# Optimization experiments

Hardware: AMD Instinct MI355X
Metric: run time of the kernel (lower is better)

The kernel has to match this reference:

```python
import jax, jax.numpy as jnp
import numpy as np

T_SCALES = [0.0, 0.25, 0.5, 0.75, 1.0]  # ODEblock time_scales; Euler step per consecutive pair
NUM_ZEROS = 10
BETA = 0.6  # defined in ODEFunc but unused in its forward


def _odefunc(x, x0, adj, alpha, w, d, w2, d2):
    # x: [B, N, T, Fa]; adj: [N, N]; alpha: [N]; w: [Fa, Fa]; d: [Fa]; w2: [T, T]; d2: [T]
    a = jax.nn.sigmoid(alpha)[None, :, None, None]              # [1, N, 1, 1]
    xa = jnp.einsum('ij,kjln->kiln', adj, x)                    # adjacency propagation over nodes
    dc = jnp.clip(d, 0.0, 1.0)
    W = (w * dc) @ w.T                                          # [Fa, Fa]
    # NOTE: faithful to torch source: 'ijkl,mn->ijkm' has NO shared contraction
    # index => xw = (sum_l x) outer (sum_n W) — reproduced exactly.
    xw = jnp.einsum('ijkl,mn->ijkm', x, W)
    d2c = jnp.clip(d2, 0.0, 1.0)
    W2 = (w2 * d2c) @ w2.T                                      # [T, T]
    xw2 = jnp.einsum('ijkl,kn->ijnl', x, W2)                    # temporal mixing
    # f = alpha/2*xa - x + xw - x + xw2 - x + x0
    return a * 0.5 * xa - 3.0 * x + xw + xw2 + x0


def setup_inputs() -> dict:
    key = jax.random.key(0)
    k1, k2 = jax.random.split(key)
    B, N, T, F = 32, 512, 24, 64
    Fa = F + NUM_ZEROS
    x = jax.random.normal(k1, (B, N, T, F), dtype=jnp.float32)
    adj = jax.random.uniform(k2, (N, N), dtype=jnp.float32) / N  # normalized dense adjacency
    alpha = 0.8 * jnp.ones((N,), jnp.float32)                    # nn.Parameter init 0.8*ones
    w = jnp.eye(Fa, dtype=jnp.float32)                           # nn.Parameter init eye
    d = jnp.ones((Fa,), jnp.float32)                             # nn.Parameter init ones
    w2 = jnp.eye(T, dtype=jnp.float32)
    d2 = jnp.ones((T,), jnp.float32)
    return {"x": x, "adj": adj, "alpha": alpha, "w": w, "d": d, "w2": w2, "d2": d2}


def reference(x, adj, alpha, w, d, w2, d2):
    B, N, T, F = x.shape
    if F == 64:
        x_aug = jnp.concatenate(
            [x, jnp.zeros((B, N, T, NUM_ZEROS), dtype=x.dtype)], axis=3)
    else:
        x_aug = x
    x0 = jax.lax.stop_gradient(x_aug)  # set_x0 uses clone().detach()
    # Euler odeint with two time points does one step: z = x + dt * f(x).
    # Original loop restarts from x_aug each iteration, so f is constant.
    f = _odefunc(x_aug, x0, adj, alpha, w, d, w2, d2)
    z = x_aug
    for i in range(len(T_SCALES) - 1):
        dt = T_SCALES[i + 1] - T_SCALES[i]
        z = x_aug + dt * f  # overwrites z each iteration, as in the torch code
    return jax.nn.relu(z)
```

## Files before the change

### kernel.cpp

```cpp
#include <hip/hip_runtime.h>
#include <hip/hip_bf16.h>
#include <cstdint>
#include <cstddef>

#define B_  32
#define N_  512
#define T_  24
#define F_  64
#define FA_ 74
#define NC  1536

typedef __attribute__((ext_vector_type(8))) short short8;
typedef __attribute__((ext_vector_type(4))) float floatx4;

#define WS_ADJB 1536
#define WS_XT   132608

#define AS1(p) ((const __attribute__((address_space(1))) void*)(p))
#define AS3(p) ((__attribute__((address_space(3))) void*)(p))

__global__ __launch_bounds__(256) void params_kernel(
    const float* __restrict__ alpha, const float* __restrict__ w,
    const float* __restrict__ d, const float* __restrict__ w2,
    const float* __restrict__ d2, float* __restrict__ ws) {
  __shared__ float cs[FA_];
  int tid = threadIdx.x;
  if (tid < FA_) {
    float s = 0.f;
    for (int n = 0; n < FA_; ++n) s += w[n * FA_ + tid];
    cs[tid] = s;
  }
  __syncthreads();
  if (tid < FA_) {
    float s = 0.f;
    for (int p = 0; p < FA_; ++p) {
      float dc = fminf(fmaxf(d[p], 0.f), 1.f);
      s += w[tid * FA_ + p] * dc * cs[p];
    }
    ws[tid] = s;
  }
  for (int e = tid; e < T_ * T_; e += 256) {
    int a = e / T_, b = e % T_;
    float s = 0.f;
    for (int p = 0; p < T_; ++p) {
      float dc = fminf(fmaxf(d2[p], 0.f), 1.f);
      s += w2[a * T_ + p] * dc * w2[b * T_ + p];
    }
    ws[128 + e] = s;
  }
  for (int i = tid; i < N_; i += 256) ws[768 + i] = 1.f / (1.f + __expf(-alpha[i]));
}

__global__ __launch_bounds__(256) void convert_adj_kernel(
    const float* __restrict__ adj, float* __restrict__ ws) {
  __hip_bfloat16* adjB = (__hip_bfloat16*)(ws + WS_ADJB);
  int g = (blockIdx.x * 256 + threadIdx.x) * 4;
  float4 v = *(const float4*)&adj[g];
  ushort4 u;
  __hip_bfloat16 h;
  h = __float2bfloat16(v.x); u.x = *(unsigned short*)&h;
  h = __float2bfloat16(v.y); u.y = *(unsigned short*)&h;
  h = __float2bfloat16(v.z); u.z = *(unsigned short*)&h;
  h = __float2bfloat16(v.w); u.w = *(unsigned short*)&h;
  *(ushort4*)&adjB[g] = u;
}

__global__ __launch_bounds__(256) void transpose_x_kernel(
    const float* __restrict__ x, float* __restrict__ ws) {
  __hip_bfloat16* xT = (__hip_bfloat16*)(ws + WS_XT);
  __shared__ float tile[64 * 65];
  int tid = threadIdx.x;
  int b = blockIdx.z;
  int c0 = blockIdx.x * 64;
  int k0 = blockIdx.y * 64;
#pragma unroll
  for (int it = 0; it < 4; ++it) {
    int g = it * 256 + tid;
    int k = g >> 4, c4 = g & 15;
    float4 v = *(const float4*)&x[((size_t)(b * N_ + k0 + k)) * NC + c0 + c4 * 4];
    tile[k * 65 + c4 * 4 + 0] = v.x;
    tile[k * 65 + c4 * 4 + 1] = v.y;
    tile[k * 65 + c4 * 4 + 2] = v.z;
    tile[k * 65 + c4 * 4 + 3] = v.w;
  }
  __syncthreads();
#pragma unroll
  for (int it = 0; it < 4; ++it) {
    int h = it * 256 + tid;
    int c = h >> 4, k4 = h & 15;
    ushort4 u;
    __hip_bfloat16 hb;
    hb = __float2bfloat16(tile[(k4 * 4 + 0) * 65 + c]); u.x = *(unsigned short*)&hb;
    hb = __float2bfloat16(tile[(k4 * 4 + 1) * 65 + c]); u.y = *(unsigned short*)&hb;
    hb = __float2bfloat16(tile[(k4 * 4 + 2) * 65 + c]); u.z = *(unsigned short*)&hb;
    hb = __float2bfloat16(tile[(k4 * 4 + 3) * 65 + c]); u.w = *(unsigned short*)&hb;
    *(ushort4*)&xT[((size_t)b * NC + c0 + c) * 512 + k0 + k4 * 4] = u;
  }
}

__global__ __launch_bounds__(256) void pass1_kernel(
    const float* __restrict__ x, const float* __restrict__ ws, float* __restrict__ out) {
  __shared__ float xs[4 * T_ * FA_];
  __shared__ float Ss[4 * T_];
  __shared__ float rsWs[80];
  int tid = threadIdx.x;
  int blk = blockIdx.x;
  int b = blk >> 7;
  int i0 = (blk & 127) << 2;
  const float* xb = x + (size_t)(b * N_ + i0) * NC;

  if (tid < FA_) rsWs[tid] = ws[tid];
#pragma unroll
  for (int it = 0; it < 6; ++it) {
    int g = it * 256 + tid;
    *(float4*)&xs[g * 4] = *(const float4*)&xb[g * 4];
  }
  __syncthreads();

  int node = tid >> 6, f = tid & 63;
  float xcol[24];
#pragma unroll
  for (int t = 0; t < 24; ++t) xcol[t] = xs[node * 1536 + t * 64 + f];
  __syncthreads();

  float S[24];
#pragma unroll
  for (int t = 0; t < 24; ++t) S[t] = xcol[t];
#pragma unroll
  for (int off = 32; off >= 1; off >>= 1) {
#pragma unroll
    for (int t = 0; t < 24; ++t) S[t] += __shfl_xor(S[t], off, 64);
  }
  if ((tid & 63) == 0) {
#pragma unroll
    for (int t = 0; t < 24; ++t) Ss[node * 24 + t] = S[t];
  }

  const float* __restrict__ W2p = ws + 128;
  float accv[24];
#pragma unroll
  for (int to = 0; to < 24; ++to) {
    float a = 0.f;
#pragma unroll
    for (int tp = 0; tp < 24; ++tp) a += xcol[tp] * W2p[to * 24 + tp];
    accv[to] = a;
  }
  float rsWf = rsWs[f];
#pragma unroll
  for (int t = 0; t < 24; ++t) {
    float val = 0.5f * xcol[t] + 0.25f * S[t] * rsWf + 0.25f * accv[t];
    xs[node * 1776 + t * 74 + f] = val;
  }
  __syncthreads();

#pragma unroll
  for (int it = 0; it < 4; ++it) {
    int e = it * 256 + tid;
    if (e < 960) {
      int nd = e / 240;
      int rem = e - nd * 240;
      int t = rem / 10;
      int m = rem - t * 10;
      float val = 0.25f * Ss[nd * 24 + t] * rsWs[64 + m];
      xs[nd * 1776 + t * 74 + 64 + m] = fmaxf(val, 0.f);
    }
  }
  __syncthreads();

  float* outb = out + (size_t)(b * N_ + i0) * 1776;
#pragma unroll
  for (int it = 0; it < 7; ++it) {
    int g = it * 256 + tid;
    if (g < 1776) *(float4*)&outb[g * 4] = *(float4*)&xs[g * 4];
  }
}

__global__ __launch_bounds__(256) void gemm_kernel(
    const float* __restrict__ ws, float* __restrict__ out) {
  const unsigned short* adjB = (const unsigned short*)(ws + WS_ADJB);
  const unsigned short* xT   = (const unsigned short*)(ws + WS_XT);
  __shared__ short As[128 * 32];
  __shared__ short Bs[128 * 32];

  int tid = threadIdx.x;
  int b  = blockIdx.z;
  int i0 = blockIdx.y * 128;
  int c0 = blockIdx.x * 128;
  int wave = tid >> 6, lane = tid & 63;
  int mw = (wave & 1) * 64, nw = (wave >> 1) * 64;
  int l15 = lane & 15, l4 = lane >> 4;

  floatx4 acc[4][4];
#pragma unroll
  for (int mt = 0; mt < 4; ++mt)
#pragma unroll
    for (int nt = 0; nt < 4; ++nt) acc[mt][nt] = (floatx4){0.f, 0.f, 0.f, 0.f};

  const size_t bRow = (size_t)b * NC;
  for (int k0 = 0; k0 < 512; k0 += 32) {
#pragma unroll
    for (int rep = 0; rep < 2; ++rep) {
      int chunk = rep * 256 + tid;
      int r = chunk >> 2;
      int k8 = (chunk & 3) * 8;
      __builtin_amdgcn_global_load_lds(AS1(adjB + (size_t)(i0 + r) * 512 + k0 + k8),
                                       AS3(&As[chunk * 8]), 16, 0, 0);
      __builtin_amdgcn_global_load_lds(AS1(xT + (bRow + c0 + r) * 512 + k0 + k8),
                                       AS3(&Bs[chunk * 8]), 16, 0, 0);
    }
    __syncthreads();

    short8 af[4], bf[4];
#pragma unroll
    for (int mt = 0; mt < 4; ++mt)
      af[mt] = *(const short8*)&As[(mw + mt * 16 + l15) * 32 + l4 * 8];
#pragma unroll
    for (int nt = 0; nt < 4; ++nt)
      bf[nt] = *(const short8*)&Bs[(nw + nt * 16 + l15) * 32 + l4 * 8];
#pragma unroll
    for (int mt = 0; mt < 4; ++mt)
#pragma unroll
      for (int nt = 0; nt < 4; ++nt)
        acc[mt][nt] = __builtin_amdgcn_mfma_f32_16x16x32_bf16(af[mt], bf[nt], acc[mt][nt], 0, 0, 0);
    __syncthreads();
  }

  float coeff[4][4];
#pragma unroll
  for (int mt = 0; mt < 4; ++mt)
#pragma unroll
    for (int r = 0; r < 4; ++r)
      coeff[mt][r] = 0.125f * ws[768 + i0 + mw + mt * 16 + l4 * 4 + r];

#pragma unroll
  for (int mt = 0; mt < 4; ++mt) {
#pragma unroll
    for (int nt = 0; nt < 4; ++nt) {
      int col = c0 + nw + nt * 16 + l15;
      int t = col >> 6, f = col & 63;
#pragma unroll
      for (int r = 0; r < 4; ++r) {
        int row = i0 + mw + mt * 16 + l4 * 4 + r;
        size_t o = ((size_t)(b * N_ + row) * T_ + t) * FA_ + f;
        float val = out[o] + coeff[mt][r] * acc[mt][nt][r];
        out[o] = fmaxf(val, 0.f);
      }
    }
  }
}

extern "C" void kernel_launch(void* const* d_in, const int* in_sizes, int n_in,
                              void* d_out, int out_size, void* d_ws, size_t ws_size,
                              hipStream_t stream) {
  const float* x     = (const float*)d_in[0];
  const float* adj   = (const float*)d_in[1];
  const float* alpha = (const float*)d_in[2];
  const float* w     = (const float*)d_in[3];
  const float* d     = (const float*)d_in[4];
  const float* w2    = (const float*)d_in[5];
  const float* d2    = (const float*)d_in[6];
  float* out = (float*)d_out;
  float* ws  = (float*)d_ws;

  hipLaunchKernelGGL(params_kernel, dim3(1), dim3(256), 0, stream,
                     alpha, w, d, w2, d2, ws);
  hipLaunchKernelGGL(convert_adj_kernel, dim3(256), dim3(256), 0, stream, adj, ws);
  hipLaunchKernelGGL(transpose_x_kernel, dim3(24, 8, B_), dim3(256), 0, stream, x, ws);
  hipLaunchKernelGGL(pass1_kernel, dim3(B_ * (N_ / 4)), dim3(256), 0, stream, x, ws, out);
  hipLaunchKernelGGL(gemm_kernel, dim3(12, 4, B_), dim3(256), 0, stream, ws, out);
}
```

Baseline: 345.5 us.

## Fuse x transpose with elementwise pass and stage bf16 epilogue buffer

Merges the x transpose and the per-node elementwise pass into one prep kernel, so x is read once, converted to bf16 and written both transposed for the GEMM and as a bf16 epilogue term. The sigmoid(alpha)/8 row scale is folded into the bf16 adjacency conversion, which removes the coefficient load in the GEMM epilogue. When the workspace is large enough, the GEMM epilogue reads a bf16 E buffer instead of doing a read-modify-write on the fp32 output. This cuts global traffic but adds bf16 rounding to the residual terms, and launches fewer blocks (32x32) per prep pass.

```diff
diff --git a/kernel.cpp b/kernel.cpp
--- a/kernel.cpp
+++ b/kernel.cpp
@@ -9,15 +9,26 @@
 #define F_  64
 #define FA_ 74
 #define NC  1536
+#define NCF 1776
 
 typedef __attribute__((ext_vector_type(8))) short short8;
 typedef __attribute__((ext_vector_type(4))) float floatx4;
 
-#define WS_ADJB 1536
+#define WS_ADJ  1536
 #define WS_XT   132608
+#define WS_E    12715520
+#define WS_BYTES_NEEDED (27264512ULL * 4ULL)
 
 #define AS1(p) ((const __attribute__((address_space(1))) void*)(p))
 #define AS3(p) ((__attribute__((address_space(3))) void*)(p))
+
+__device__ __forceinline__ unsigned short f2b(float v) {
+  __hip_bfloat16 h = __float2bfloat16(v);
+  return *(unsigned short*)&h;
+}
+__device__ __forceinline__ float b2f(unsigned short u) {
+  return __uint_as_float(((unsigned)u) << 16);
+}
 
 __global__ __launch_bounds__(256) void params_kernel(
     const float* __restrict__ alpha, const float* __restrict__ w,
@@ -53,131 +64,132 @@
 
 __global__ __launch_bounds__(256) void convert_adj_kernel(
     const float* __restrict__ adj, float* __restrict__ ws) {
-  __hip_bfloat16* adjB = (__hip_bfloat16*)(ws + WS_ADJB);
+  unsigned short* adjM = (unsigned short*)(ws + WS_ADJ);
   int g = (blockIdx.x * 256 + threadIdx.x) * 4;
+  int i = g >> 9;
+  float s = 0.125f * ws[768 + i];
   float4 v = *(const float4*)&adj[g];
   ushort4 u;
-  __hip_bfloat16 h;
-  h = __float2bfloat16(v.x); u.x = *(unsigned short*)&h;
-  h = __float2bfloat16(v.y); u.y = *(unsigned short*)&h;
-  h = __float2bfloat16(v.z); u.z = *(unsigned short*)&h;
-  h = __float2bfloat16(v.w); u.w = *(unsigned short*)&h;
-  *(ushort4*)&adjB[g] = u;
-}
-
-__global__ __launch_bounds__(256) void transpose_x_kernel(
-    const float* __restrict__ x, float* __restrict__ ws) {
-  __hip_bfloat16* xT = (__hip_bfloat16*)(ws + WS_XT);
-  __shared__ float tile[64 * 65];
+  u.x = f2b(s * v.x); u.y = f2b(s * v.y); u.z = f2b(s * v.z); u.w = f2b(s * v.w);
+  *(ushort4*)&adjM[g] = u;
+}
+
+template <bool EPATH>
+__global__ __launch_bounds__(256) void prep_kernel(
+    const float* __restrict__ x, float* __restrict__ ws, float* __restrict__ out) {
+  __shared__ __align__(16) unsigned short xsh[16 * NC];
+  __shared__ __align__(16) float ebuf[4 * NCF];
+  unsigned short* eh = (unsigned short*)ebuf;
+
   int tid = threadIdx.x;
-  int b = blockIdx.z;
-  int c0 = blockIdx.x * 64;
-  int k0 = blockIdx.y * 64;
-#pragma unroll
-  for (int it = 0; it < 4; ++it) {
+  int b = blockIdx.y;
+  int i0 = blockIdx.x * 16;
+  const float* xb = x + ((size_t)(b * N_ + i0)) * NC;
+
+#pragma unroll
+  for (int it = 0; it < 24; ++it) {
     int g = it * 256 + tid;
-    int k = g >> 4, c4 = g & 15;
-    float4 v = *(const float4*)&x[((size_t)(b * N_ + k0 + k)) * NC + c0 + c4 * 4];
-    tile[k * 65 + c4 * 4 + 0] = v.x;
-    tile[k * 65 + c4 * 4 + 1] = v.y;
-    tile[k * 65 + c4 * 4 + 2] = v.z;
-    tile[k * 65 + c4 * 4 + 3] = v.w;
+    float4 v = *(const float4*)&xb[g * 4];
+    ushort4 u;
+    u.x = f2b(v.x); u.y = f2b(v.y); u.z = f2b(v.z); u.w = f2b(v.w);
+    *(ushort4*)&xsh[g * 4] = u;
   }
   __syncthreads();
-#pragma unroll
-  for (int it = 0; it < 4; ++it) {
-    int h = it * 256 + tid;
-    int c = h >> 4, k4 = h & 15;
-    ushort4 u;
-    __hip_bfloat16 hb;
-    hb = __float2bfloat16(tile[(k4 * 4 + 0) * 65 + c]); u.x = *(unsigned short*)&hb;
-    hb = __float2bfloat16(tile[(k4 * 4 + 1) * 65 + c]); u.y = *(unsigned short*)&hb;
-    hb = __float2bfloat16(tile[(k4 * 4 + 2) * 65 + c]); u.z = *(unsigned short*)&hb;
-    hb = __float2bfloat16(tile[(k4 * 4 + 3) * 65 + c]); u.w = *(unsigned short*)&hb;
-    *(ushort4*)&xT[((size_t)b * NC + c0 + c) * 512 + k0 + k4 * 4] = u;
-  }
-}
-
-__global__ __launch_bounds__(256) void pass1_kernel(
-    const float* __restrict__ x, const float* __restrict__ ws, float* __restrict__ out) {
-  __shared__ float xs[4 * T_ * FA_];
-  __shared__ float Ss[4 * T_];
-  __shared__ float rsWs[80];
-  int tid = threadIdx.x;
-  int blk = blockIdx.x;
-  int b = blk >> 7;
-  int i0 = (blk & 127) << 2;
-  const float* xb = x + (size_t)(b * N_ + i0) * NC;
-
-  if (tid < FA_) rsWs[tid] = ws[tid];
-#pragma unroll
-  for (int it = 0; it < 6; ++it) {
-    int g = it * 256 + tid;
-    *(float4*)&xs[g * 4] = *(const float4*)&xb[g * 4];
-  }
-  __syncthreads();
-
-  int node = tid >> 6, f = tid & 63;
-  float xcol[24];
-#pragma unroll
-  for (int t = 0; t < 24; ++t) xcol[t] = xs[node * 1536 + t * 64 + f];
-  __syncthreads();
-
-  float S[24];
-#pragma unroll
-  for (int t = 0; t < 24; ++t) S[t] = xcol[t];
-#pragma unroll
-  for (int off = 32; off >= 1; off >>= 1) {
-#pragma unroll
-    for (int t = 0; t < 24; ++t) S[t] += __shfl_xor(S[t], off, 64);
-  }
-  if ((tid & 63) == 0) {
-#pragma unroll
-    for (int t = 0; t < 24; ++t) Ss[node * 24 + t] = S[t];
-  }
-
+
+  unsigned short* xT = (unsigned short*)(ws + WS_XT) + (size_t)b * NC * 512;
+#pragma unroll
+  for (int j = 0; j < 6; ++j) {
+    int c = j * 256 + tid;
+    unsigned vv[8];
+#pragma unroll
+    for (int k2 = 0; k2 < 8; ++k2) {
+      unsigned lo = xsh[(2 * k2) * NC + c];
+      unsigned hi = xsh[(2 * k2 + 1) * NC + c];
+      vv[k2] = lo | (hi << 16);
+    }
+    uint4 w0; w0.x = vv[0]; w0.y = vv[1]; w0.z = vv[2]; w0.w = vv[3];
+    uint4 w1; w1.x = vv[4]; w1.y = vv[5]; w1.z = vv[6]; w1.w = vv[7];
+    *(uint4*)&xT[(size_t)c * 512 + i0] = w0;
+    *(uint4*)&xT[(size_t)c * 512 + i0 + 8] = w1;
+  }
+
+  int wave = tid >> 6, lane = tid & 63;
   const float* __restrict__ W2p = ws + 128;
-  float accv[24];
-#pragma unroll
-  for (int to = 0; to < 24; ++to) {
-    float a = 0.f;
-#pragma unroll
-    for (int tp = 0; tp < 24; ++tp) a += xcol[tp] * W2p[to * 24 + tp];
-    accv[to] = a;
-  }
-  float rsWf = rsWs[f];
-#pragma unroll
-  for (int t = 0; t < 24; ++t) {
-    float val = 0.5f * xcol[t] + 0.25f * S[t] * rsWf + 0.25f * accv[t];
-    xs[node * 1776 + t * 74 + f] = val;
-  }
-  __syncthreads();
-
-#pragma unroll
-  for (int it = 0; it < 4; ++it) {
-    int e = it * 256 + tid;
-    if (e < 960) {
-      int nd = e / 240;
-      int rem = e - nd * 240;
-      int t = rem / 10;
-      int m = rem - t * 10;
-      float val = 0.25f * Ss[nd * 24 + t] * rsWs[64 + m];
-      xs[nd * 1776 + t * 74 + 64 + m] = fmaxf(val, 0.f);
-    }
-  }
-  __syncthreads();
-
-  float* outb = out + (size_t)(b * N_ + i0) * 1776;
-#pragma unroll
-  for (int it = 0; it < 7; ++it) {
-    int g = it * 256 + tid;
-    if (g < 1776) *(float4*)&outb[g * 4] = *(float4*)&xs[g * 4];
-  }
-}
-
+  float rsw4 = 0.25f * ws[lane];
+  float rswA = (lane < 10) ? 0.25f * ws[64 + lane] : 0.f;
+
+  for (int p = 0; p < 4; ++p) {
+    int node = p * 4 + wave;
+    float xcol[24];
+#pragma unroll
+    for (int t = 0; t < 24; ++t) xcol[t] = b2f(xsh[node * NC + t * 64 + lane]);
+    float S[24];
+#pragma unroll
+    for (int t = 0; t < 24; ++t) S[t] = xcol[t];
+#pragma unroll
+    for (int off = 32; off >= 1; off >>= 1) {
+#pragma unroll
+      for (int t = 0; t < 24; ++t) S[t] += __shfl_xor(S[t], off, 64);
+    }
+    float accv[24];
+#pragma unroll
+    for (int to = 0; to < 24; ++to) {
+      float a = 0.f;
+#pragma unroll
+      for (int tp = 0; tp < 24; ++tp) a += xcol[tp] * W2p[to * 24 + tp];
+      accv[to] = a;
+    }
+#pragma unroll
+    for (int t = 0; t < 24; ++t) {
+      float ev = 0.5f * xcol[t] + 0.25f * accv[t] + S[t] * rsw4;
+      if (EPATH) eh[wave * NCF + t * 74 + lane] = f2b(ev);
+      else       ebuf[wave * NCF + t * 74 + lane] = ev;
+    }
+#pragma unroll
+    for (int t = 0; t < 24; ++t) {
+      if (lane < 10) {
+        float av = fmaxf(S[t] * rswA, 0.f);
+        if (EPATH) eh[wave * NCF + t * 74 + 64 + lane] = f2b(av);
+        else       ebuf[wave * NCF + t * 74 + 64 + lane] = av;
+      }
+    }
+    __syncthreads();
+    if (EPATH) {
+      unsigned short* Eg = (unsigned short*)(ws + WS_E) +
+                           ((size_t)(b * N_ + i0 + p * 4)) * NCF;
+      const uint4* src = (const uint4*)eh;
+      uint4* dst = (uint4*)Eg;
+#pragma unroll
+      for (int j = 0; j < 4; ++j) {
+        int idx = j * 256 + tid;
+        if (idx < 888) dst[idx] = src[idx];
+      }
+      float* ob = out + ((size_t)(b * N_ + i0 + p * 4)) * NCF;
+#pragma unroll
+      for (int j = 0; j < 4; ++j) {
+        int e = j * 256 + tid;
+        if (e < 960) {
+          int nd = e / 240, rem = e - nd * 240;
+          int t = rem / 10, m = rem - t * 10;
+          ob[(size_t)nd * NCF + t * 74 + 64 + m] = b2f(eh[nd * NCF + t * 74 + 64 + m]);
+        }
+      }
+    } else {
+      float* og = out + ((size_t)(b * N_ + i0 + p * 4)) * NCF;
+#pragma unroll
+      for (int j = 0; j < 7; ++j) {
+        int idx = j * 256 + tid;
+        if (idx < 1776) ((float4*)og)[idx] = ((const float4*)ebuf)[idx];
+      }
+    }
+    __syncthreads();
+  }
+}
+
+template <bool EPATH>
 __global__ __launch_bounds__(256) void gemm_kernel(
     const float* __restrict__ ws, float* __restrict__ out) {
-  const unsigned short* adjB = (const unsigned short*)(ws + WS_ADJB);
+  const unsigned short* adjM = (const unsigned short*)(ws + WS_ADJ);
   const unsigned short* xT   = (const unsigned short*)(ws + WS_XT);
   __shared__ short As[128 * 32];
   __shared__ short Bs[128 * 32];
@@ -203,7 +215,7 @@
       int chunk = rep * 256 + tid;
       int r = chunk >> 2;
       int k8 = (chunk & 3) * 8;
-      __builtin_amdgcn_global_load_lds(AS1(adjB + (size_t)(i0 + r) * 512 + k0 + k8),
+      __builtin_amdgcn_global_load_lds(AS1(adjM + (size_t)(i0 + r) * 512 + k0 + k8),
                                        AS3(&As[chunk * 8]), 16, 0, 0);
       __builtin_amdgcn_global_load_lds(AS1(xT + (bRow + c0 + r) * 512 + k0 + k8),
                                        AS3(&Bs[chunk * 8]), 16, 0, 0);
@@ -225,24 +237,21 @@
     __syncthreads();
   }
 
-  float coeff[4][4];
-#pragma unroll
-  for (int mt = 0; mt < 4; ++mt)
-#pragma unroll
-    for (int r = 0; r < 4; ++r)
-      coeff[mt][r] = 0.125f * ws[768 + i0 + mw + mt * 16 + l4 * 4 + r];
-
+  const unsigned short* Eb = (const unsigned short*)(ws + WS_E) + (size_t)b * N_ * NCF;
 #pragma unroll
   for (int mt = 0; mt < 4; ++mt) {
 #pragma unroll
     for (int nt = 0; nt < 4; ++nt) {
       int col = c0 + nw + nt * 16 + l15;
       int t = col >> 6, f = col & 63;
+      int cofs = t * 74 + f;
 #pragma unroll
       for (int r = 0; r < 4; ++r) {
         int row = i0 + mw + mt * 16 + l4 * 4 + r;
-        size_t o = ((size_t)(b * N_ + row) * T_ + t) * FA_ + f;
-        float val = out[o] + coeff[mt][r] * acc[mt][nt][r];
+        size_t o = (size_t)(b * N_ + row) * NCF + cofs;
+        float val;
+        if (EPATH) val = acc[mt][nt][r] + b2f(Eb[(size_t)row * NCF + cofs]);
+        else       val = out[o] + acc[mt][nt][r];
         out[o] = fmaxf(val, 0.f);
       }
     }
@@ -265,7 +274,12 @@
   hipLaunchKernelGGL(params_kernel, dim3(1), dim3(256), 0, stream,
                      alpha, w, d, w2, d2, ws);
   hipLaunchKernelGGL(convert_adj_kernel, dim3(256), dim3(256), 0, stream, adj, ws);
-  hipLaunchKernelGGL(transpose_x_kernel, dim3(24, 8, B_), dim3(256), 0, stream, x, ws);
-  hipLaunchKernelGGL(pass1_kernel, dim3(B_ * (N_ / 4)), dim3(256), 0, stream, x, ws, out);
-  hipLaunchKernelGGL(gemm_kernel, dim3(12, 4, B_), dim3(256), 0, stream, ws, out);
-}
+
+  if (ws_size >= WS_BYTES_NEEDED) {
+    hipLaunchKernelGGL((prep_kernel<true>), dim3(32, 32), dim3(256), 0, stream, x, ws, out);
+    hipLaunchKernelGGL((gemm_kernel<true>), dim3(12, 4, B_), dim3(256), 0, stream, ws, out);
+  } else {
+    hipLaunchKernelGGL((prep_kernel<false>), dim3(32, 32), dim3(256), 0, stream, x, ws, out);
+    hipLaunchKernelGGL((gemm_kernel<false>), dim3(12, 4, B_), dim3(256), 0, stream, ws, out);
+  }
+}
```

Measured after the change: 391.8 us. 13.4% more time.
